# Performance work log

Measured on AMD Instinct MI355X. Metric: run time of the kernel, lower is better.

Reference implementation:

```python
import jax, jax.numpy as jnp
from jax import lax
import numpy as np

SEQ, BATCH, IN, HID = 512, 256, 248, 1024


def setup_inputs() -> dict:
    key = jax.random.key(0)
    ks = jax.random.split(key, 9)
    s_in = 1.0 / np.sqrt(HID)  # pytorch default init scale for RNN/Linear
    x = jax.random.normal(ks[0], (SEQ, BATCH, IN), dtype=jnp.float32)
    W_ih = jax.random.uniform(ks[1], (HID, IN), jnp.float32, -s_in, s_in)
    b_ih = jax.random.uniform(ks[2], (HID,), jnp.float32, -s_in, s_in)
    W_hh = jax.random.uniform(ks[3], (HID, HID), jnp.float32, -s_in, s_in)
    b_hh = jax.random.uniform(ks[4], (HID,), jnp.float32, -s_in, s_in)
    W_out = jax.random.uniform(ks[5], (1, HID), jnp.float32, -s_in, s_in)
    b_out = jax.random.uniform(ks[6], (1,), jnp.float32, -s_in, s_in)
    w_r = jax.random.uniform(ks[7], (1, 1), jnp.float32, -1.0, 1.0)
    b_r = jax.random.uniform(ks[8], (1,), jnp.float32, -1.0, 1.0)
    return {"x": x, "W_ih": W_ih, "b_ih": b_ih, "W_hh": W_hh, "b_hh": b_hh,
            "W_out": W_out, "b_out": b_out, "w_r": w_r, "b_r": b_r}


def reference(x, W_ih, b_ih, W_hh, b_hh, W_out, b_out, w_r, b_r):
    # x: (T, B, IN) time-major, like torch nn.RNN default.
    T, B, _ = x.shape
    H = W_hh.shape[0]
    # Precompute input projection for all timesteps: (T, B, H)
    xproj = jnp.einsum('tbi,hi->tbh', x, W_ih) + b_ih + b_hh

    def rnn_step(h, xp):
        h_new = jnp.tanh(xp + h @ W_hh.T)
        return h_new, h_new

    h0 = jnp.zeros((B, H), dtype=x.dtype)
    _, hs = lax.scan(rnn_step, h0, xproj)  # hs: (T, B, H)

    # Output logits for all timesteps: (T, B, 1)
    z = jnp.einsum('tbh,oh->tbo', hs, W_out) + b_out

    # o_0 = sigmoid(z_0); o_t = sigmoid(z_t + recurr(o_{t-1}))
    o0 = jax.nn.sigmoid(z[0])

    def out_step(o_prev, zt):
        o = jax.nn.sigmoid(zt + o_prev @ w_r.T + b_r)
        return o, o

    _, os = lax.scan(out_step, o0, z[1:])
    o_all = jnp.concatenate([o0[None], os], axis=0)  # (T, B, 1)
    return o_all[:, :, 0].T  # (B, T), matching oFinal
```

## Files before the change

kernel.cpp:

```cpp
#include <hip/hip_runtime.h>

#define T_SEQ 512
#define NB    256
#define NIN   248
#define NH    1024

typedef __attribute__((ext_vector_type(8))) short          short8;
typedef __attribute__((ext_vector_type(4))) float          f32x4;
typedef __attribute__((ext_vector_type(4))) unsigned int   uint4v;
typedef __attribute__((ext_vector_type(4))) float          float4v;
typedef unsigned long long u64;

#define AS_RELAXED __ATOMIC_RELAXED
#define AS_AGENT   __HIP_MEMORY_SCOPE_AGENT

__device__ __forceinline__ unsigned short f2bf(float f){
  unsigned int u = __float_as_uint(f);
  u += 0x7FFFu + ((u >> 16) & 1u);
  return (unsigned short)(u >> 16);
}
__device__ __forceinline__ unsigned pk2(float lo, float hi){
  return (unsigned)f2bf(lo) | ((unsigned)f2bf(hi) << 16);
}
__device__ __forceinline__ float tanh_fast(float v){
  float e = __expf(2.0f * v);
  return 1.0f - 2.0f / (e + 1.0f);
}

__device__ __forceinline__ void barrier_lds(){
  asm volatile("s_waitcnt lgkmcnt(0)" ::: "memory");
  __builtin_amdgcn_s_barrier();
  __builtin_amdgcn_sched_barrier(0);
}

__launch_bounds__(256, 1)
__global__ void rnn_scan_kernel(const float* __restrict__ x,
                                const float* __restrict__ W_ih,
                                const float* __restrict__ b_ih,
                                const float* __restrict__ W_hh,
                                const float* __restrict__ b_hh,
                                const float* __restrict__ W_out,
                                unsigned short* __restrict__ hbuf,
                                float* __restrict__ z,
                                unsigned int* __restrict__ bar)
{
  __shared__ alignas(16) unsigned short h_frag[2048 * 8];
  __shared__ alignas(16) unsigned short x_frag[512 * 8];
  __shared__ alignas(8)  unsigned short h_out[4 * 256];
  __shared__ float z_hist[T_SEQ * 16];

  const int tid    = threadIdx.x;
  const int wg     = blockIdx.x;
  const int r16    = wg & 15;
  const int bg     = (r16 & 7) * 2 + (r16 >> 3);
  const int jg     = wg >> 4;
  const int b_base = bg * 16;
  const int l      = tid & 63;
  const int wv     = tid >> 6;
  const int n      = l & 15;
  const int quad   = l >> 4;
  const int j      = jg * 64 + wv * 16 + n;

  unsigned short* h0 = hbuf;
  unsigned short* h1 = hbuf + (size_t)NB * NH;
  unsigned int* flags = bar + bg * 64;

  short8 whh[32];
  #pragma unroll
  for (int kt = 0; kt < 32; ++kt){
    const float* p = W_hh + (size_t)j * NH + kt * 32 + quad * 8;
    float4v a = *(const float4v*)p;
    float4v b = *(const float4v*)(p + 4);
    short8 v;
    v[0]=(short)f2bf(a[0]); v[1]=(short)f2bf(a[1]); v[2]=(short)f2bf(a[2]); v[3]=(short)f2bf(a[3]);
    v[4]=(short)f2bf(b[0]); v[5]=(short)f2bf(b[1]); v[6]=(short)f2bf(b[2]); v[7]=(short)f2bf(b[3]);
    whh[kt] = v;
  }
  short8 wih[8];
  #pragma unroll
  for (int kt = 0; kt < 8; ++kt){
    short8 v = {0,0,0,0,0,0,0,0};
    if (!(kt == 7 && quad == 3)){
      const float* p = W_ih + (size_t)j * NIN + kt * 32 + quad * 8;
      float4v a = *(const float4v*)p;
      float4v b = *(const float4v*)(p + 4);
      v[0]=(short)f2bf(a[0]); v[1]=(short)f2bf(a[1]); v[2]=(short)f2bf(a[2]); v[3]=(short)f2bf(a[3]);
      v[4]=(short)f2bf(b[0]); v[5]=(short)f2bf(b[1]); v[6]=(short)f2bf(b[2]); v[7]=(short)f2bf(b[3]);
    }
    wih[kt] = v;
  }
  const float bias  = b_ih[j] + b_hh[j];
  const float woutj = W_out[j];

  #pragma unroll
  for (int i = 0; i < 32; ++i) z_hist[tid + i * 256] = 0.f;
  {
    int r = tid >> 4, c = (tid & 15) * 4;
    __hip_atomic_store((u64*)&h0[(size_t)(b_base + r) * NH + jg * 64 + c],
                       0ull, AS_RELAXED, AS_AGENT);
    int tt = jg * 32 + (tid >> 3);
    int bb = (tid & 7) * 2;
    __hip_atomic_store(&z[(size_t)tt * NB + b_base + bb],     0.f, AS_RELAXED, AS_AGENT);
    __hip_atomic_store(&z[(size_t)tt * NB + b_base + bb + 1], 0.f, AS_RELAXED, AS_AGENT);
  }
  asm volatile("s_waitcnt vmcnt(0)" ::: "memory");
  if (l == 0)
    __hip_atomic_store(&flags[jg * 4 + wv], 1u, AS_RELAXED, AS_AGENT);

  const int xslot_kt[2] = { tid >> 6, (tid + 256) >> 6 };
  const int xslot_l2[2] = { tid & 63, tid & 63 };
  float4v xr[2][2];
  bool    xvalid[2];
  #pragma unroll
  for (int i = 0; i < 2; ++i){
    int kt = xslot_kt[i], l2 = xslot_l2[i];
    int b = b_base + (l2 & 15), k = kt * 32 + (l2 >> 4) * 8;
    xvalid[i] = !(kt == 7 && (l2 >> 4) == 3);
    if (xvalid[i]){
      const float* p = x + ((size_t)0 * NB + b) * NIN + k;
      xr[i][0] = *(const float4v*)p;
      xr[i][1] = *(const float4v*)(p + 4);
    }
  }

  unsigned spec = 0;

  for (int t = 0; t < T_SEQ; ++t){
    const unsigned short* hp = (t & 1) ? h1 : h0;
    unsigned short*       hn = (t & 1) ? h0 : h1;
    const int tn = (t + 1 < T_SEQ) ? t + 1 : t;

    if (!__all((int)(spec >= (unsigned)(t + 1)))){
      unsigned v;
      do {
        __builtin_amdgcn_s_sleep(1);
        v = __hip_atomic_load(&flags[l], AS_RELAXED, AS_AGENT);
      } while (!__all((int)(v >= (unsigned)(t + 1))));
    }
    __builtin_amdgcn_sched_barrier(0);

    u64 hw0[8], hw1[8];
    #pragma unroll
    for (int i = 0; i < 8; ++i){
      int slot = tid + i * 256;
      int kt = slot >> 6, l2 = slot & 63;
      const u64* src = (const u64*)(hp
          + (size_t)(b_base + (l2 & 15)) * NH + kt * 32 + (l2 >> 4) * 8);
      hw0[i] = __hip_atomic_load(src,     AS_RELAXED, AS_AGENT);
      hw1[i] = __hip_atomic_load(src + 1, AS_RELAXED, AS_AGENT);
    }
    #pragma unroll
    for (int i = 0; i < 2; ++i){
      uint4v v = {0u,0u,0u,0u};
      if (xvalid[i]){
        v[0] = pk2(xr[i][0][0], xr[i][0][1]);
        v[1] = pk2(xr[i][0][2], xr[i][0][3]);
        v[2] = pk2(xr[i][1][0], xr[i][1][1]);
        v[3] = pk2(xr[i][1][2], xr[i][1][3]);
      }
      *(uint4v*)&x_frag[(tid + i * 256) * 8] = v;
    }
    #pragma unroll
    for (int i = 0; i < 4; ++i){
      u64* dst = (u64*)&h_frag[(tid + i * 256) * 8];
      dst[0] = hw0[i]; dst[1] = hw1[i];
    }
    barrier_lds();

    f32x4 a0 = {bias, bias, bias, bias};
    f32x4 a1 = {0.f, 0.f, 0.f, 0.f};
    f32x4 a2 = {0.f, 0.f, 0.f, 0.f};
    f32x4 a3 = {0.f, 0.f, 0.f, 0.f};
    #pragma unroll
    for (int kt = 0; kt < 16; kt += 4){
      short8 q0 = *(const short8*)&h_frag[((kt + 0) * 64 + l) * 8];
      short8 q1 = *(const short8*)&h_frag[((kt + 1) * 64 + l) * 8];
      short8 q2 = *(const short8*)&h_frag[((kt + 2) * 64 + l) * 8];
      short8 q3 = *(const short8*)&h_frag[((kt + 3) * 64 + l) * 8];
      a0 = __builtin_amdgcn_mfma_f32_16x16x32_bf16(q0, whh[kt + 0], a0, 0, 0, 0);
      a1 = __builtin_amdgcn_mfma_f32_16x16x32_bf16(q1, whh[kt + 1], a1, 0, 0, 0);
      a2 = __builtin_amdgcn_mfma_f32_16x16x32_bf16(q2, whh[kt + 2], a2, 0, 0, 0);
      a3 = __builtin_amdgcn_mfma_f32_16x16x32_bf16(q3, whh[kt + 3], a3, 0, 0, 0);
    }
    __builtin_amdgcn_sched_barrier(0);

    #pragma unroll
    for (int i = 4; i < 8; ++i){
      u64* dst = (u64*)&h_frag[(tid + i * 256) * 8];
      dst[0] = hw0[i]; dst[1] = hw1[i];
    }
    barrier_lds();

    #pragma unroll
    for (int kt = 16; kt < 32; kt += 4){
      short8 q0 = *(const short8*)&h_frag[((kt + 0) * 64 + l) * 8];
      short8 q1 = *(const short8*)&h_frag[((kt + 1) * 64 + l) * 8];
      short8 q2 = *(const short8*)&h_frag[((kt + 2) * 64 + l) * 8];
      short8 q3 = *(const short8*)&h_frag[((kt + 3) * 64 + l) * 8];
      a0 = __builtin_amdgcn_mfma_f32_16x16x32_bf16(q0, whh[kt + 0], a0, 0, 0, 0);
      a1 = __builtin_amdgcn_mfma_f32_16x16x32_bf16(q1, whh[kt + 1], a1, 0, 0, 0);
      a2 = __builtin_amdgcn_mfma_f32_16x16x32_bf16(q2, whh[kt + 2], a2, 0, 0, 0);
      a3 = __builtin_amdgcn_mfma_f32_16x16x32_bf16(q3, whh[kt + 3], a3, 0, 0, 0);
    }
    #pragma unroll
    for (int kt = 0; kt < 8; kt += 4){
      short8 q0 = *(const short8*)&x_frag[((kt + 0) * 64 + l) * 8];
      short8 q1 = *(const short8*)&x_frag[((kt + 1) * 64 + l) * 8];
      short8 q2 = *(const short8*)&x_frag[((kt + 2) * 64 + l) * 8];
      short8 q3 = *(const short8*)&x_frag[((kt + 3) * 64 + l) * 8];
      a0 = __builtin_amdgcn_mfma_f32_16x16x32_bf16(q0, wih[kt + 0], a0, 0, 0, 0);
      a1 = __builtin_amdgcn_mfma_f32_16x16x32_bf16(q1, wih[kt + 1], a1, 0, 0, 0);
      a2 = __builtin_amdgcn_mfma_f32_16x16x32_bf16(q2, wih[kt + 2], a2, 0, 0, 0);
      a3 = __builtin_amdgcn_mfma_f32_16x16x32_bf16(q3, wih[kt + 3], a3, 0, 0, 0);
    }

    float hv[4];
    #pragma unroll
    for (int i = 0; i < 4; ++i){
      hv[i] = tanh_fast(a0[i] + a1[i] + a2[i] + a3[i]);
      h_out[wv * 256 + (quad * 4 + i) * 16 + n] = f2bf(hv[i]);
    }
    {
      int r = l >> 2, c = (l & 3) * 4;
      u64 v = *(const u64*)&h_out[wv * 256 + r * 16 + c];
      __hip_atomic_store((u64*)&hn[(size_t)(b_base + r) * NH
                         + jg * 64 + wv * 16 + c], v, AS_RELAXED, AS_AGENT);
    }
    asm volatile("s_waitcnt vmcnt(0)" ::: "memory");
    if (l == 0)
      __hip_atomic_store(&flags[jg * 4 + wv], (unsigned)(t + 2),
                         AS_RELAXED, AS_AGENT);
    __builtin_amdgcn_sched_barrier(0);

    #pragma unroll
    for (int i = 0; i < 2; ++i){
      if (xvalid[i]){
        int kt = xslot_kt[i], l2 = xslot_l2[i];
        int b = b_base + (l2 & 15), k = kt * 32 + (l2 >> 4) * 8;
        const float* p = x + ((size_t)tn * NB + b) * NIN + k;
        xr[i][0] = *(const float4v*)p;
        xr[i][1] = *(const float4v*)(p + 4);
      }
    }
    float sv[4];
    #pragma unroll
    for (int i = 0; i < 4; ++i) sv[i] = hv[i] * woutj;
    #pragma unroll
    for (int m = 1; m < 16; m <<= 1){
      #pragma unroll
      for (int i = 0; i < 4; ++i) sv[i] += __shfl_xor(sv[i], m, 64);
    }
    if (n == 0){
      #pragma unroll
      for (int i = 0; i < 4; ++i) atomicAdd(&z_hist[t * 16 + quad * 4 + i], sv[i]);
    }
    spec = __hip_atomic_load(&flags[l], AS_RELAXED, AS_AGENT);
  }

  __syncthreads();
  #pragma unroll
  for (int i = 0; i < 32; ++i){
    int idx = tid + i * 256;
    int tt = idx >> 4, bb = idx & 15;
    atomicAdd(&z[(size_t)tt * NB + b_base + bb], z_hist[idx]);
  }
}

__global__ void out_scan_kernel(const float* __restrict__ z,
                                const float* __restrict__ b_out,
                                const float* __restrict__ w_r,
                                const float* __restrict__ b_r,
                                float* __restrict__ out)
{
  int b = threadIdx.x;
  float bo = b_out[0], wr = w_r[0], br = b_r[0];
  float o = 0.f;
  for (int t = 0; t < T_SEQ; ++t){
    float pre = z[(size_t)t * NB + b] + bo;
    if (t > 0) pre += wr * o + br;
    o = 1.0f / (1.0f + __expf(-pre));
    out[(size_t)b * T_SEQ + t] = o;
  }
}

extern "C" void kernel_launch(void* const* d_in, const int* in_sizes, int n_in,
                              void* d_out, int out_size, void* d_ws, size_t ws_size,
                              hipStream_t stream)
{
  (void)in_sizes; (void)n_in; (void)out_size; (void)ws_size;
  const float* x     = (const float*)d_in[0];
  const float* W_ih  = (const float*)d_in[1];
  const float* b_ih  = (const float*)d_in[2];
  const float* W_hh  = (const float*)d_in[3];
  const float* b_hh  = (const float*)d_in[4];
  const float* W_out = (const float*)d_in[5];
  const float* b_out = (const float*)d_in[6];
  const float* w_r   = (const float*)d_in[7];
  const float* b_r   = (const float*)d_in[8];
  float* out = (float*)d_out;

  unsigned short* hbuf = (unsigned short*)d_ws;
  float* z = (float*)((char*)d_ws + 2 * (size_t)NB * NH * sizeof(unsigned short));
  unsigned int* bar = (unsigned int*)((char*)d_ws
                        + 2 * (size_t)NB * NH * sizeof(unsigned short)
                        + (size_t)T_SEQ * NB * sizeof(float));

  hipMemsetAsync(bar, 0, 16 * 64 * sizeof(unsigned int), stream);

  rnn_scan_kernel<<<dim3(256), dim3(256), 0, stream>>>(
      x, W_ih, b_ih, W_hh, b_hh, W_out, hbuf, z, bar);

  out_scan_kernel<<<dim3(1), dim3(256), 0, stream>>>(z, b_out, w_r, b_r, out);
}
```

Before: 2.436 ms.

## Drop split-phase LDS staging, use two accumulators, remove spin sleep

Removes the two-phase h staging that let the first half of the MFMAs overlap with writing the second half into LDS; now all 8 h fragments are written before a single barrier. The four independent accumulator chains become two, the s_sleep in the flag spin loop is dropped, and an extra LDS barrier is added after the flag store, with the next-step x prefetch moved after the z reduction. The aim is a shorter per-step critical path and faster wakeup in the latency-bound recurrent loop, at the cost of less overlap, longer dependent MFMA chains, more memory traffic from busy polling, and an extra barrier.

```diff
diff --git a/kernel.cpp b/kernel.cpp
--- a/kernel.cpp
+++ b/kernel.cpp
@@ -128,12 +128,10 @@
   for (int t = 0; t < T_SEQ; ++t){
     const unsigned short* hp = (t & 1) ? h1 : h0;
     unsigned short*       hn = (t & 1) ? h0 : h1;
-    const int tn = (t + 1 < T_SEQ) ? t + 1 : t;
 
     if (!__all((int)(spec >= (unsigned)(t + 1)))){
       unsigned v;
       do {
-        __builtin_amdgcn_s_sleep(1);
         v = __hip_atomic_load(&flags[l], AS_RELAXED, AS_AGENT);
       } while (!__all((int)(v >= (unsigned)(t + 1))));
     }
@@ -161,63 +159,33 @@
       *(uint4v*)&x_frag[(tid + i * 256) * 8] = v;
     }
     #pragma unroll
-    for (int i = 0; i < 4; ++i){
+    for (int i = 0; i < 8; ++i){
       u64* dst = (u64*)&h_frag[(tid + i * 256) * 8];
       dst[0] = hw0[i]; dst[1] = hw1[i];
     }
     barrier_lds();
 
-    f32x4 a0 = {bias, bias, bias, bias};
-    f32x4 a1 = {0.f, 0.f, 0.f, 0.f};
-    f32x4 a2 = {0.f, 0.f, 0.f, 0.f};
-    f32x4 a3 = {0.f, 0.f, 0.f, 0.f};
-    #pragma unroll
-    for (int kt = 0; kt < 16; kt += 4){
-      short8 q0 = *(const short8*)&h_frag[((kt + 0) * 64 + l) * 8];
-      short8 q1 = *(const short8*)&h_frag[((kt + 1) * 64 + l) * 8];
-      short8 q2 = *(const short8*)&h_frag[((kt + 2) * 64 + l) * 8];
-      short8 q3 = *(const short8*)&h_frag[((kt + 3) * 64 + l) * 8];
-      a0 = __builtin_amdgcn_mfma_f32_16x16x32_bf16(q0, whh[kt + 0], a0, 0, 0, 0);
-      a1 = __builtin_amdgcn_mfma_f32_16x16x32_bf16(q1, whh[kt + 1], a1, 0, 0, 0);
-      a2 = __builtin_amdgcn_mfma_f32_16x16x32_bf16(q2, whh[kt + 2], a2, 0, 0, 0);
-      a3 = __builtin_amdgcn_mfma_f32_16x16x32_bf16(q3, whh[kt + 3], a3, 0, 0, 0);
-    }
-    __builtin_amdgcn_sched_barrier(0);
-
-    #pragma unroll
-    for (int i = 4; i < 8; ++i){
-      u64* dst = (u64*)&h_frag[(tid + i * 256) * 8];
-      dst[0] = hw0[i]; dst[1] = hw1[i];
-    }
-    barrier_lds();
-
-    #pragma unroll
-    for (int kt = 16; kt < 32; kt += 4){
-      short8 q0 = *(const short8*)&h_frag[((kt + 0) * 64 + l) * 8];
-      short8 q1 = *(const short8*)&h_frag[((kt + 1) * 64 + l) * 8];
-      short8 q2 = *(const short8*)&h_frag[((kt + 2) * 64 + l) * 8];
-      short8 q3 = *(const short8*)&h_frag[((kt + 3) * 64 + l) * 8];
-      a0 = __builtin_amdgcn_mfma_f32_16x16x32_bf16(q0, whh[kt + 0], a0, 0, 0, 0);
-      a1 = __builtin_amdgcn_mfma_f32_16x16x32_bf16(q1, whh[kt + 1], a1, 0, 0, 0);
-      a2 = __builtin_amdgcn_mfma_f32_16x16x32_bf16(q2, whh[kt + 2], a2, 0, 0, 0);
-      a3 = __builtin_amdgcn_mfma_f32_16x16x32_bf16(q3, whh[kt + 3], a3, 0, 0, 0);
-    }
-    #pragma unroll
-    for (int kt = 0; kt < 8; kt += 4){
-      short8 q0 = *(const short8*)&x_frag[((kt + 0) * 64 + l) * 8];
-      short8 q1 = *(const short8*)&x_frag[((kt + 1) * 64 + l) * 8];
-      short8 q2 = *(const short8*)&x_frag[((kt + 2) * 64 + l) * 8];
-      short8 q3 = *(const short8*)&x_frag[((kt + 3) * 64 + l) * 8];
-      a0 = __builtin_amdgcn_mfma_f32_16x16x32_bf16(q0, wih[kt + 0], a0, 0, 0, 0);
-      a1 = __builtin_amdgcn_mfma_f32_16x16x32_bf16(q1, wih[kt + 1], a1, 0, 0, 0);
-      a2 = __builtin_amdgcn_mfma_f32_16x16x32_bf16(q2, wih[kt + 2], a2, 0, 0, 0);
-      a3 = __builtin_amdgcn_mfma_f32_16x16x32_bf16(q3, wih[kt + 3], a3, 0, 0, 0);
+    f32x4 acc0 = {bias, bias, bias, bias};
+    f32x4 acc1 = {0.f, 0.f, 0.f, 0.f};
+    #pragma unroll
+    for (int kt = 0; kt < 32; kt += 2){
+      short8 a0 = *(const short8*)&h_frag[(kt * 64 + l) * 8];
+      short8 a1 = *(const short8*)&h_frag[((kt + 1) * 64 + l) * 8];
+      acc0 = __builtin_amdgcn_mfma_f32_16x16x32_bf16(a0, whh[kt],     acc0, 0, 0, 0);
+      acc1 = __builtin_amdgcn_mfma_f32_16x16x32_bf16(a1, whh[kt + 1], acc1, 0, 0, 0);
+    }
+    #pragma unroll
+    for (int kt = 0; kt < 8; kt += 2){
+      short8 a0 = *(const short8*)&x_frag[(kt * 64 + l) * 8];
+      short8 a1 = *(const short8*)&x_frag[((kt + 1) * 64 + l) * 8];
+      acc0 = __builtin_amdgcn_mfma_f32_16x16x32_bf16(a0, wih[kt],     acc0, 0, 0, 0);
+      acc1 = __builtin_amdgcn_mfma_f32_16x16x32_bf16(a1, wih[kt + 1], acc1, 0, 0, 0);
     }
 
     float hv[4];
     #pragma unroll
     for (int i = 0; i < 4; ++i){
-      hv[i] = tanh_fast(a0[i] + a1[i] + a2[i] + a3[i]);
+      hv[i] = tanh_fast(acc0[i] + acc1[i]);
       h_out[wv * 256 + (quad * 4 + i) * 16 + n] = f2bf(hv[i]);
     }
     {
@@ -231,17 +199,8 @@
       __hip_atomic_store(&flags[jg * 4 + wv], (unsigned)(t + 2),
                          AS_RELAXED, AS_AGENT);
     __builtin_amdgcn_sched_barrier(0);
-
-    #pragma unroll
-    for (int i = 0; i < 2; ++i){
-      if (xvalid[i]){
-        int kt = xslot_kt[i], l2 = xslot_l2[i];
-        int b = b_base + (l2 & 15), k = kt * 32 + (l2 >> 4) * 8;
-        const float* p = x + ((size_t)tn * NB + b) * NIN + k;
-        xr[i][0] = *(const float4v*)p;
-        xr[i][1] = *(const float4v*)(p + 4);
-      }
-    }
+    barrier_lds();
+
     float sv[4];
     #pragma unroll
     for (int i = 0; i < 4; ++i) sv[i] = hv[i] * woutj;
@@ -253,6 +212,19 @@
     if (n == 0){
       #pragma unroll
       for (int i = 0; i < 4; ++i) atomicAdd(&z_hist[t * 16 + quad * 4 + i], sv[i]);
+    }
+    {
+      int tn = (t + 1 < T_SEQ) ? t + 1 : t;
+      #pragma unroll
+      for (int i = 0; i < 2; ++i){
+        if (xvalid[i]){
+          int kt = xslot_kt[i], l2 = xslot_l2[i];
+          int b = b_base + (l2 & 15), k = kt * 32 + (l2 >> 4) * 8;
+          const float* p = x + ((size_t)tn * NB + b) * NIN + k;
+          xr[i][0] = *(const float4v*)p;
+          xr[i][1] = *(const float4v*)(p + 4);
+        }
+      }
     }
     spec = __hip_atomic_load(&flags[l], AS_RELAXED, AS_AGENT);
   }
```

Result: no change. 2.465 ms (+1.2%).
